# Optimization experiments

Measured on AMD Instinct MI355X. Metric: run time of the kernel, lower is better.

Reference implementation:

```python
import jax, jax.numpy as jnp
from jax import lax
import numpy as np


def setup_inputs() -> dict:
    key = jax.random.key(0)
    k1, k2, k3, k4, k5 = jax.random.split(key, 5)
    bs, m, v, L, P = 2, 16, 16, 40320, 32
    preds = jax.random.normal(k1, (bs, m, v, L), dtype=jnp.float32)
    target = jax.random.normal(k2, (bs, v, L), dtype=jnp.float32)
    weights = jax.random.uniform(k3, (L,), dtype=jnp.float32)
    scale = jax.random.uniform(k4, (v,), dtype=jnp.float32)
    # binary-ish patch masks over grid points (float, as in the torch buffer)
    masks = (jax.random.uniform(k5, (P, L)) < 0.25).astype(jnp.float32)
    return {"preds": preds, "target": target, "weights": weights,
            "scale": scale, "masks": masks, "beta": 1}


def _energy_score(x, y, m, beta):
    # x: (bs, m, D) ensemble, y: (bs, D) observation
    diff = x - y[:, None, :]
    a = jnp.sqrt(jnp.sum(diff * diff, axis=-1))            # (bs, m)
    score_a = jnp.mean(jnp.sum(a ** beta, axis=-1)) / m
    # pairwise distances via Gram trick (cdist p=2)
    sq = jnp.sum(x * x, axis=-1)                            # (bs, m)
    g = jnp.einsum('bid,bjd->bij', x, x)                    # (bs, m, m)
    d2 = jnp.maximum(sq[:, :, None] + sq[:, None, :] - 2.0 * g, 0.0)
    pos = d2 > 0
    d = jnp.where(pos, jnp.sqrt(jnp.where(pos, d2, 1.0)), 0.0)
    score_b = jnp.mean(jnp.sum(d ** beta, axis=(1, 2))) / (2 * m * (m - 1))
    return score_a - score_b


def reference(preds, target, weights, scale, masks, beta):
    beta = float(beta)
    bs, m, v, L = preds.shape
    # buffer scaling as in forward()
    p = preds * scale[None, None, :, None] * weights        # (bs, m, v, L)
    t = target * scale[None, :, None] * weights             # (bs, v, L)

    def body(acc, mask):
        # rearrange 'bs m v latlon -> bs m (latlon v)'
        x = (p * mask).transpose(0, 1, 3, 2).reshape(bs, m, L * v)
        y = (t * mask).transpose(0, 2, 1).reshape(bs, L * v)
        return acc + _energy_score(x, y, m, beta), None

    total, _ = lax.scan(body, jnp.float32(0.0), masks)
    return total
```

## Files before the change

### kernel.cpp

```cpp
#include <hip/hip_runtime.h>
#include <math.h>

#define BS 2
#define M 16
#define V 16
#define NROWB 136
#define NROWS 272
#define PMASK 32
#define NPB 630
#define NE 8704
#define PBSTRIDE 8704
#define SPLIT 30
#define QPB 21

typedef __attribute__((ext_vector_type(8))) short bf16x8;
typedef __attribute__((ext_vector_type(4))) float f32x4;
typedef __attribute__((ext_vector_type(4))) unsigned int u32x4;

#define VMW(n) asm volatile("s_waitcnt vmcnt(" #n ")" ::: "memory")

static __device__ __forceinline__ unsigned short f2bf(float x) {
    unsigned int u = __float_as_uint(x);
    unsigned int r = (u + 0x7FFFu + ((u >> 16) & 1u)) >> 16;
    return (unsigned short)r;
}

static __device__ __forceinline__ void k1_stage(
    const float* __restrict__ preds, float* __restrict__ dst,
    int b, int v0, int l0, int L, int lane, int wave)
{
#pragma unroll
    for (int n = 0; n < 2; ++n) {
        int r0 = wave * 8 + n * 4;
        int r = r0 + (lane >> 4);
        int grow = b * 256 + (r >> 1) * 16 + v0 + (r & 1);
        const float* g = preds + (size_t)grow * L + l0 + (lane & 15) * 4;
        __builtin_amdgcn_global_load_lds(
            (const __attribute__((address_space(1))) unsigned int*)g,
            (__attribute__((address_space(3))) unsigned int*)(dst + r0 * 64),
            16, 0, 0);
    }
}

template<int W>
static __device__ __forceinline__ void k1_chunk(
    const float* __restrict__ xsb,
    const float* __restrict__ targ,
    const float* __restrict__ scl,
    float wl,
    int v0, int lane, float* __restrict__ acc)
{
    const int base = (W == 0) ? 0 : 34 * W - 16;
    const int npair = (W == 0) ? 18 : 34;
    const int aoff = (W == 0) ? 16 : 0;

#pragma unroll
    for (int vc = 0; vc < 2; ++vc) {
        const int v = v0 + vc;
        float s = scl[v] * wl;
        float x[M];
#pragma unroll
        for (int i = 0; i < M; ++i)
            x[i] = xsb[(i * 2 + vc) * 64 + lane] * s;
        if (W == 0) {
            float y = targ[v] * s;
#pragma unroll
            for (int i = 0; i < M; ++i) {
                float d = x[i] - y;
                acc[i] = fmaf(d, d, acc[i]);
            }
        }
        int k = 0;
#pragma unroll
        for (int i = 0; i < M; ++i) {
#pragma unroll
            for (int j = i + 1; j < M; ++j) {
                if (k >= base && k < base + npair) {
                    float d = x[i] - x[j];
                    acc[aoff + k - base] = fmaf(d, d, acc[aoff + k - base]);
                }
                ++k;
            }
        }
    }
}

__global__ __launch_bounds__(256, 2)
void k1_fused(const float* __restrict__ preds, const float* __restrict__ target,
              const float* __restrict__ weights, const float* __restrict__ scale,
              const float* __restrict__ masks, float* __restrict__ partial,
              float* __restrict__ out, int L)
{
    __shared__ float xs[4][2048];
    unsigned short* sld = (unsigned short*)&xs[0][0];

    const int t = (int)threadIdx.x;
    const int lane = t & 63, wave = t >> 6;
    const int pb = (int)blockIdx.x;
    const int b  = (int)blockIdx.y;
    const int l0 = pb * 64;

    if (pb == 0 && b == 0 && t == 0) out[0] = 0.0f;

    const size_t Ls = (size_t)L;

    const float wl = weights[l0 + lane];
    float scl[V];
#pragma unroll
    for (int v = 0; v < V; ++v) scl[v] = scale[v];
    float targ[V];
    if (wave == 0) {
#pragma unroll
        for (int v = 0; v < V; ++v)
            targ[v] = target[(size_t)(b * V + v) * Ls + l0 + lane];
    }
    __builtin_amdgcn_sched_barrier(0);

    k1_stage(preds, &xs[0][0], b, 0, l0, L, lane, wave);
    k1_stage(preds, &xs[1][0], b, 2, l0, L, lane, wave);
    k1_stage(preds, &xs[2][0], b, 4, l0, L, lane, wave);

    float acc[34];
#pragma unroll
    for (int r = 0; r < 34; ++r) acc[r] = 0.0f;

#pragma unroll
    for (int s = 0; s < 8; ++s) {
        if (s < 6)      { VMW(4); }
        else if (s == 6){ VMW(2); }
        else            { VMW(0); }
        __builtin_amdgcn_s_barrier();
        __builtin_amdgcn_sched_barrier(0);
        if (s < 5)
            k1_stage(preds, &xs[(s + 3) & 3][0], b, (s + 3) * 2, l0, L, lane, wave);
        const float* xsb = &xs[s & 3][0];
        switch (wave) {
            case 0: k1_chunk<0>(xsb, targ, scl, wl, s * 2, lane, acc); break;
            case 1: k1_chunk<1>(xsb, targ, scl, wl, s * 2, lane, acc); break;
            case 2: k1_chunk<2>(xsb, targ, scl, wl, s * 2, lane, acc); break;
            default: k1_chunk<3>(xsb, targ, scl, wl, s * 2, lane, acc); break;
        }
    }

    ((unsigned int*)sld)[136 * 32 + t] = 0;

#pragma unroll
    for (int r = 0; r < 34; ++r) {
        const int R = 34 * wave + r;
        sld[R * 64 + (lane ^ ((R & 7) << 3))] = f2bf(acc[r]);
    }
    __syncthreads();

    const int ntile = (wave == 3) ? 3 : 2;
    f32x4 pacc[3][2];
#pragma unroll
    for (int ti = 0; ti < 3; ++ti)
#pragma unroll
        for (int pt = 0; pt < 2; ++pt)
            pacc[ti][pt] = (f32x4){0.f, 0.f, 0.f, 0.f};

#pragma unroll
    for (int ks = 0; ks < 2; ++ks) {
        bf16x8 bfr[2];
#pragma unroll
        for (int pt = 0; pt < 2; ++pt) {
            const float* mp = masks + (size_t)(pt * 16 + (lane & 15)) * Ls
                            + l0 + ks * 32 + (lane >> 4) * 8;
            u32x4 m0 = *(const u32x4*)mp;
            u32x4 m1 = *(const u32x4*)(mp + 4);
            union { unsigned int u[4]; bf16x8 v; } bb;
            bb.u[0] = __builtin_amdgcn_perm(m0.y, m0.x, 0x07060302);
            bb.u[1] = __builtin_amdgcn_perm(m0.w, m0.z, 0x07060302);
            bb.u[2] = __builtin_amdgcn_perm(m1.y, m1.x, 0x07060302);
            bb.u[3] = __builtin_amdgcn_perm(m1.w, m1.z, 0x07060302);
            bfr[pt] = bb.v;
        }
#pragma unroll
        for (int ti = 0; ti < 3; ++ti) {
            if (ti >= ntile) continue;
            const int tile = (ti == 2) ? 8 : (wave + ti * 4);
            const bf16x8 a = *(const bf16x8*)&sld[
                (tile * 16 + (lane & 15)) * 64 +
                ((ks * 32 + (lane >> 4) * 8) ^ ((lane & 7) << 3))];
            pacc[ti][0] = __builtin_amdgcn_mfma_f32_16x16x32_bf16(
                a, bfr[0], pacc[ti][0], 0, 0, 0);
            pacc[ti][1] = __builtin_amdgcn_mfma_f32_16x16x32_bf16(
                a, bfr[1], pacc[ti][1], 0, 0, 0);
        }
    }

    float* P = partial + (size_t)(pb * 2 + b) * (NROWB * PMASK);
#pragma unroll
    for (int ti = 0; ti < 3; ++ti) {
        if (ti >= ntile) continue;
        const int tile = (ti == 2) ? 8 : (wave + ti * 4);
#pragma unroll
        for (int pt = 0; pt < 2; ++pt)
#pragma unroll
            for (int reg = 0; reg < 4; ++reg) {
                const int row = tile * 16 + (lane >> 4) * 4 + reg;
                if (row < NROWB)
                    P[row * 32 + pt * 16 + (lane & 15)] = pacc[ti][pt][reg];
            }
    }
}

__global__ __launch_bounds__(256, 2)
void k3a_reduce(const float* __restrict__ P, float* __restrict__ P2)
{
    const int t = (int)threadIdx.x;
    const int e = (int)blockIdx.x * 256 + t;
    const int spl = (int)blockIdx.y;

    const float* p = P + (size_t)(spl * QPB) * PBSTRIDE + e;
    float a[7];
#pragma unroll
    for (int j = 0; j < 7; ++j) a[j] = 0.f;
    for (int q = 0; q < QPB; q += 7) {
#pragma unroll
        for (int j = 0; j < 7; ++j)
            a[j] += p[(size_t)(q + j) * PBSTRIDE];
    }
    P2[(size_t)spl * NE + e] =
        ((a[0] + a[1]) + (a[2] + a[3])) + ((a[4] + a[5]) + a[6]);
}

__global__ __launch_bounds__(256, 2)
void k3b_finalize(const float* __restrict__ P2, const int* __restrict__ beta_p,
                  float* __restrict__ out)
{
    const int t = (int)threadIdx.x;
    const int e = (int)blockIdx.x * 256 + t;

    float a0 = 0.f, a1 = 0.f, a2 = 0.f;
#pragma unroll
    for (int q = 0; q < SPLIT; q += 3) {
        a0 += P2[(size_t)(q    ) * NE + e];
        a1 += P2[(size_t)(q + 1) * NE + e];
        a2 += P2[(size_t)(q + 2) * NE + e];
    }
    float d2 = fmaxf((a0 + a1) + a2, 0.0f);
    float beta = (float)beta_p[0];
    float d = (beta == 1.0f) ? sqrtf(d2) : powf(d2, 0.5f * beta);

    const float wa = 1.0f / (float)(BS * M);
    const float wb = -1.0f / (float)(BS * M * (M - 1));
    const int row_g = e >> 5;
    const int local = row_g % NROWB;
    float sum = ((local < M) ? wa : wb) * d;

    const int lane = t & 63, wv = t >> 6;
#pragma unroll
    for (int off = 32; off > 0; off >>= 1)
        sum += __shfl_down(sum, off, 64);
    __shared__ float red[4];
    if (lane == 0) red[wv] = sum;
    __syncthreads();
    if (t == 0)
        atomicAdd(out, red[0] + red[1] + red[2] + red[3]);
}

extern "C" void kernel_launch(void* const* d_in, const int* in_sizes, int n_in,
                              void* d_out, int out_size, void* d_ws, size_t ws_size,
                              hipStream_t stream)
{
    const float* preds   = (const float*)d_in[0];
    const float* target  = (const float*)d_in[1];
    const float* weights = (const float*)d_in[2];
    const float* scale   = (const float*)d_in[3];
    const float* masks   = (const float*)d_in[4];
    const int*   beta    = (const int*)d_in[5];
    float* out = (float*)d_out;

    int L = in_sizes[2];

    float* partial = (float*)d_ws;
    size_t p_bytes = (size_t)NPB * 2 * NROWB * PMASK * sizeof(float);
    float* partial2 = (float*)((char*)d_ws + ((p_bytes + 255) & ~(size_t)255));

    dim3 g1(NPB, BS);
    k1_fused<<<g1, 256, 0, stream>>>(preds, target, weights, scale, masks,
                                     partial, out, L);

    dim3 g3a(NE / 256, SPLIT);
    k3a_reduce<<<g3a, 256, 0, stream>>>(partial, partial2);

    k3b_finalize<<<NE / 256, 256, 0, stream>>>(partial2, beta, out);
}
```

Measured before the change: 152.2 us.

## Process 128 grid points per block with two accumulator sets and staged target

Each block of the fused pairwise-distance kernel now covers 128 longitude points instead of 64, with two register accumulator sets per thread and the MFMA mask projection run twice into the same partial accumulators. This halves the block count and the per-block partial outputs, which shrinks the downstream reduction (SPLIT halved). Target values are now staged into LDS with async global-to-LDS loads instead of per-lane register loads. In exchange, LDS use doubles and register pressure rises (68 accumulators), which may lower occupancy or cause spills under the 2-blocks-per-CU launch bound.

```diff
diff --git a/kernel.cpp b/kernel.cpp
--- a/kernel.cpp
+++ b/kernel.cpp
@@ -7,10 +7,10 @@
 #define NROWB 136
 #define NROWS 272
 #define PMASK 32
-#define NPB 630
+#define NPB 315
 #define NE 8704
 #define PBSTRIDE 8704
-#define SPLIT 30
+#define SPLIT 15
 #define QPB 21
 
 typedef __attribute__((ext_vector_type(8))) short bf16x8;
@@ -30,14 +30,30 @@
     int b, int v0, int l0, int L, int lane, int wave)
 {
 #pragma unroll
-    for (int n = 0; n < 2; ++n) {
-        int r0 = wave * 8 + n * 4;
-        int r = r0 + (lane >> 4);
+    for (int n = 0; n < 4; ++n) {
+        int r0 = wave * 8 + n * 2;
+        int r = r0 + (lane >> 5);
         int grow = b * 256 + (r >> 1) * 16 + v0 + (r & 1);
-        const float* g = preds + (size_t)grow * L + l0 + (lane & 15) * 4;
+        const float* g = preds + (size_t)grow * L + l0 + (lane & 31) * 4;
         __builtin_amdgcn_global_load_lds(
             (const __attribute__((address_space(1))) unsigned int*)g,
-            (__attribute__((address_space(3))) unsigned int*)(dst + r0 * 64),
+            (__attribute__((address_space(3))) unsigned int*)(dst + r0 * 128),
+            16, 0, 0);
+    }
+}
+
+static __device__ __forceinline__ void k1_stage_t(
+    const float* __restrict__ target, float* __restrict__ dst,
+    int b, int l0, int L, int lane, int wave)
+{
+#pragma unroll
+    for (int n = 0; n < 2; ++n) {
+        int r0 = wave * 4 + n * 2;
+        int r = r0 + (lane >> 5);
+        const float* g = target + (size_t)(b * V + r) * L + l0 + (lane & 31) * 4;
+        __builtin_amdgcn_global_load_lds(
+            (const __attribute__((address_space(1))) unsigned int*)g,
+            (__attribute__((address_space(3))) unsigned int*)(dst + r0 * 128),
             16, 0, 0);
     }
 }
@@ -45,10 +61,9 @@
 template<int W>
 static __device__ __forceinline__ void k1_chunk(
     const float* __restrict__ xsb,
-    const float* __restrict__ targ,
+    const float* __restrict__ tl,
     const float* __restrict__ scl,
-    float wl,
-    int v0, int lane, float* __restrict__ acc)
+    float wl, int v0, int lcol, float* __restrict__ acc)
 {
     const int base = (W == 0) ? 0 : 34 * W - 16;
     const int npair = (W == 0) ? 18 : 34;
@@ -61,9 +76,9 @@
         float x[M];
 #pragma unroll
         for (int i = 0; i < M; ++i)
-            x[i] = xsb[(i * 2 + vc) * 64 + lane] * s;
+            x[i] = xsb[(i * 2 + vc) * 128 + lcol] * s;
         if (W == 0) {
-            float y = targ[v] * s;
+            float y = tl[v * 128 + lcol] * s;
 #pragma unroll
             for (int i = 0; i < M; ++i) {
                 float d = x[i] - y;
@@ -91,43 +106,40 @@
               const float* __restrict__ masks, float* __restrict__ partial,
               float* __restrict__ out, int L)
 {
-    __shared__ float xs[4][2048];
+    __shared__ float xs[4][4096];
+    __shared__ float tl[16 * 128];
     unsigned short* sld = (unsigned short*)&xs[0][0];
 
     const int t = (int)threadIdx.x;
     const int lane = t & 63, wave = t >> 6;
     const int pb = (int)blockIdx.x;
     const int b  = (int)blockIdx.y;
-    const int l0 = pb * 64;
+    const int l0 = pb * 128;
 
     if (pb == 0 && b == 0 && t == 0) out[0] = 0.0f;
 
     const size_t Ls = (size_t)L;
 
-    const float wl = weights[l0 + lane];
+    const float wlA = weights[l0 + lane];
+    const float wlB = weights[l0 + 64 + lane];
     float scl[V];
 #pragma unroll
     for (int v = 0; v < V; ++v) scl[v] = scale[v];
-    float targ[V];
-    if (wave == 0) {
-#pragma unroll
-        for (int v = 0; v < V; ++v)
-            targ[v] = target[(size_t)(b * V + v) * Ls + l0 + lane];
-    }
     __builtin_amdgcn_sched_barrier(0);
 
+    k1_stage_t(target, tl, b, l0, L, lane, wave);
     k1_stage(preds, &xs[0][0], b, 0, l0, L, lane, wave);
     k1_stage(preds, &xs[1][0], b, 2, l0, L, lane, wave);
     k1_stage(preds, &xs[2][0], b, 4, l0, L, lane, wave);
 
-    float acc[34];
-#pragma unroll
-    for (int r = 0; r < 34; ++r) acc[r] = 0.0f;
+    float accA[34], accB[34];
+#pragma unroll
+    for (int r = 0; r < 34; ++r) { accA[r] = 0.0f; accB[r] = 0.0f; }
 
 #pragma unroll
     for (int s = 0; s < 8; ++s) {
-        if (s < 6)      { VMW(4); }
-        else if (s == 6){ VMW(2); }
+        if (s < 6)      { VMW(8); }
+        else if (s == 6){ VMW(4); }
         else            { VMW(0); }
         __builtin_amdgcn_s_barrier();
         __builtin_amdgcn_sched_barrier(0);
@@ -135,21 +147,18 @@
             k1_stage(preds, &xs[(s + 3) & 3][0], b, (s + 3) * 2, l0, L, lane, wave);
         const float* xsb = &xs[s & 3][0];
         switch (wave) {
-            case 0: k1_chunk<0>(xsb, targ, scl, wl, s * 2, lane, acc); break;
-            case 1: k1_chunk<1>(xsb, targ, scl, wl, s * 2, lane, acc); break;
-            case 2: k1_chunk<2>(xsb, targ, scl, wl, s * 2, lane, acc); break;
-            default: k1_chunk<3>(xsb, targ, scl, wl, s * 2, lane, acc); break;
+            case 0: k1_chunk<0>(xsb, tl, scl, wlA, s * 2, lane, accA);
+                    k1_chunk<0>(xsb, tl, scl, wlB, s * 2, 64 + lane, accB); break;
+            case 1: k1_chunk<1>(xsb, tl, scl, wlA, s * 2, lane, accA);
+                    k1_chunk<1>(xsb, tl, scl, wlB, s * 2, 64 + lane, accB); break;
+            case 2: k1_chunk<2>(xsb, tl, scl, wlA, s * 2, lane, accA);
+                    k1_chunk<2>(xsb, tl, scl, wlB, s * 2, 64 + lane, accB); break;
+            default: k1_chunk<3>(xsb, tl, scl, wlA, s * 2, lane, accA);
+                     k1_chunk<3>(xsb, tl, scl, wlB, s * 2, 64 + lane, accB); break;
         }
     }
 
     ((unsigned int*)sld)[136 * 32 + t] = 0;
-
-#pragma unroll
-    for (int r = 0; r < 34; ++r) {
-        const int R = 34 * wave + r;
-        sld[R * 64 + (lane ^ ((R & 7) << 3))] = f2bf(acc[r]);
-    }
-    __syncthreads();
 
     const int ntile = (wave == 3) ? 3 : 2;
     f32x4 pacc[3][2];
@@ -160,36 +169,49 @@
             pacc[ti][pt] = (f32x4){0.f, 0.f, 0.f, 0.f};
 
 #pragma unroll
-    for (int ks = 0; ks < 2; ++ks) {
-        bf16x8 bfr[2];
-#pragma unroll
-        for (int pt = 0; pt < 2; ++pt) {
-            const float* mp = masks + (size_t)(pt * 16 + (lane & 15)) * Ls
-                            + l0 + ks * 32 + (lane >> 4) * 8;
-            u32x4 m0 = *(const u32x4*)mp;
-            u32x4 m1 = *(const u32x4*)(mp + 4);
-            union { unsigned int u[4]; bf16x8 v; } bb;
-            bb.u[0] = __builtin_amdgcn_perm(m0.y, m0.x, 0x07060302);
-            bb.u[1] = __builtin_amdgcn_perm(m0.w, m0.z, 0x07060302);
-            bb.u[2] = __builtin_amdgcn_perm(m1.y, m1.x, 0x07060302);
-            bb.u[3] = __builtin_amdgcn_perm(m1.w, m1.z, 0x07060302);
-            bfr[pt] = bb.v;
-        }
-#pragma unroll
-        for (int ti = 0; ti < 3; ++ti) {
-            if (ti >= ntile) continue;
-            const int tile = (ti == 2) ? 8 : (wave + ti * 4);
-            const bf16x8 a = *(const bf16x8*)&sld[
-                (tile * 16 + (lane & 15)) * 64 +
-                ((ks * 32 + (lane >> 4) * 8) ^ ((lane & 7) << 3))];
-            pacc[ti][0] = __builtin_amdgcn_mfma_f32_16x16x32_bf16(
-                a, bfr[0], pacc[ti][0], 0, 0, 0);
-            pacc[ti][1] = __builtin_amdgcn_mfma_f32_16x16x32_bf16(
-                a, bfr[1], pacc[ti][1], 0, 0, 0);
-        }
-    }
-
-    float* P = partial + (size_t)(pb * 2 + b) * (NROWB * PMASK);
+    for (int half = 0; half < 2; ++half) {
+        const float* acc = (half == 0) ? accA : accB;
+#pragma unroll
+        for (int r = 0; r < 34; ++r) {
+            const int R = 34 * wave + r;
+            sld[R * 64 + (lane ^ ((R & 7) << 3))] = f2bf(acc[r]);
+        }
+        __syncthreads();
+
+#pragma unroll
+        for (int ks = 0; ks < 2; ++ks) {
+            bf16x8 bfr[2];
+#pragma unroll
+            for (int pt = 0; pt < 2; ++pt) {
+                const float* mp = masks + (size_t)(pt * 16 + (lane & 15)) * Ls
+                                + l0 + half * 64 + ks * 32 + (lane >> 4) * 8;
+                u32x4 m0 = *(const u32x4*)mp;
+                u32x4 m1 = *(const u32x4*)(mp + 4);
+                union { unsigned int u[4]; bf16x8 v; } bb;
+                bb.u[0] = __builtin_amdgcn_perm(m0.y, m0.x, 0x07060302);
+                bb.u[1] = __builtin_amdgcn_perm(m0.w, m0.z, 0x07060302);
+                bb.u[2] = __builtin_amdgcn_perm(m1.y, m1.x, 0x07060302);
+                bb.u[3] = __builtin_amdgcn_perm(m1.w, m1.z, 0x07060302);
+                bfr[pt] = bb.v;
+            }
+#pragma unroll
+            for (int ti = 0; ti < 3; ++ti) {
+                if (ti >= ntile) continue;
+                const int tile = (ti == 2) ? 8 : (wave + ti * 4);
+                const bf16x8 a = *(const bf16x8*)&sld[
+                    (tile * 16 + (lane & 15)) * 64 +
+                    ((ks * 32 + (lane >> 4) * 8) ^ ((lane & 7) << 3))];
+                pacc[ti][0] = __builtin_amdgcn_mfma_f32_16x16x32_bf16(
+                    a, bfr[0], pacc[ti][0], 0, 0, 0);
+                pacc[ti][1] = __builtin_amdgcn_mfma_f32_16x16x32_bf16(
+                    a, bfr[1], pacc[ti][1], 0, 0, 0);
+            }
+        }
+        if (half == 0)
+            __syncthreads();
+    }
+
+    float* P = partial + (size_t)pb * PBSTRIDE + (size_t)b * (NROWB * PMASK);
 #pragma unroll
     for (int ti = 0; ti < 3; ++ti) {
         if (ti >= ntile) continue;
@@ -275,7 +297,7 @@
     int L = in_sizes[2];
 
     float* partial = (float*)d_ws;
-    size_t p_bytes = (size_t)NPB * 2 * NROWB * PMASK * sizeof(float);
+    size_t p_bytes = (size_t)NPB * PBSTRIDE * sizeof(float);
     float* partial2 = (float*)((char*)d_ws + ((p_bytes + 255) & ~(size_t)255));
 
     dim3 g1(NPB, BS);
```

Measured after the change: 159.2 us. 1.05x slower.
